# Kernel optimization log

Hardware: AMD Instinct MI355X
Metric: run time of the kernel (lower is better)

## Reference

```python
import jax, jax.numpy as jnp
import numpy as np

DEPTH = 2   # depth
H = 8       # heads
DH = 32     # dim_head
DIM = 256   # model dim (= H*DH)
W = 2       # sliding_window_size
C = 4       # compress_block_size == selection_block_size
NSEL = 2    # num_selected_blocks
B, S = 4, 2048


def layernorm(x, g, b, eps=1e-5):
    m = x.mean(-1, keepdims=True)
    v = jnp.var(x, axis=-1, keepdims=True)
    return (x - m) * jax.lax.rsqrt(v + eps) * g + b


def msoftmax(s, mask):
    # numerically-safe masked softmax; rows with no visible key output zeros
    s = jnp.where(mask, s, -1e9)
    p = jax.nn.softmax(s, axis=-1)
    return jnp.where(jnp.any(mask, axis=-1, keepdims=True), p, 0.0)


def nsa(x, Wq, Wk, Wv, Wg, Wo):
    # Native sparse attention: compressed + top-k selected blocks + sliding window,
    # combined with per-head sigmoid gates.
    b, s, d = x.shape
    nb = s // C
    q = (x @ Wq).reshape(b, s, H, DH).transpose(0, 2, 1, 3)  # [B,H,S,DH]
    k = (x @ Wk).reshape(b, s, H, DH).transpose(0, 2, 1, 3)
    v = (x @ Wv).reshape(b, s, H, DH).transpose(0, 2, 1, 3)
    scale = DH ** -0.5
    t = jnp.arange(s)

    # ---- compressed branch: mean-pooled KV blocks, causal over fully-past blocks
    kb = k.reshape(b, H, nb, C, DH)
    vb = v.reshape(b, H, nb, C, DH)
    kc = kb.mean(3)
    vc = vb.mean(3)
    sc = jnp.einsum('bhsd,bhnd->bhsn', q, kc) * scale       # [B,H,S,nb]
    blk_end = jnp.arange(nb) * C + (C - 1)
    cmask = blk_end[None, :] <= t[:, None]                   # [S,nb]
    pc = msoftmax(sc, cmask[None, None])
    oc = jnp.einsum('bhsn,bhnd->bhsd', pc, vc)

    # ---- selection branch: own block always + top (NSEL-1) blocks by compressed score
    own = t // C                                             # [S]
    not_own = jnp.arange(nb)[None, :] != own[:, None]        # [S,nb]
    sel_scores = jnp.where(not_own[None, None], pc, -1.0)
    top_idx = jax.lax.top_k(sel_scores, NSEL - 1)[1]         # [B,H,S,NSEL-1]
    own_idx = jnp.broadcast_to(own[None, None, :, None], (b, H, s, 1))
    idx = jnp.concatenate([own_idx, top_idx], axis=-1)       # [B,H,S,NSEL]
    idxf = idx.reshape(b, H, s * NSEL, 1, 1)
    sk = jnp.take_along_axis(kb, idxf, axis=2).reshape(b, H, s, NSEL * C, DH)
    sv = jnp.take_along_axis(vb, idxf, axis=2).reshape(b, H, s, NSEL * C, DH)
    pos = (idx[..., None] * C + jnp.arange(C)).reshape(b, H, s, NSEL * C)
    fmask = pos <= t[None, None, :, None]
    sf = jnp.einsum('bhsd,bhskd->bhsk', q, sk) * scale
    pf = msoftmax(sf, fmask)
    of = jnp.einsum('bhsk,bhskd->bhsd', pf, sv)

    # ---- sliding-window branch: causal local window of W tokens (incl. self)
    off = jnp.arange(W) - (W - 1)
    wpos = t[:, None] + off[None, :]                         # [S,W]
    widx = jnp.clip(wpos, 0, s - 1)
    kw = jnp.take(k, widx.reshape(-1), axis=2).reshape(b, H, s, W, DH)
    vw = jnp.take(v, widx.reshape(-1), axis=2).reshape(b, H, s, W, DH)
    sw = jnp.einsum('bhsd,bhsjd->bhsj', q, kw) * scale
    pw = msoftmax(sw, (wpos >= 0)[None, None])
    ow = jnp.einsum('bhsj,bhsjd->bhsd', pw, vw)

    # ---- gated combine + output projection
    g = jax.nn.sigmoid(x @ Wg).reshape(b, s, 3, H).transpose(0, 3, 1, 2)  # [B,H,S,3]
    o = g[..., 0:1] * oc + g[..., 1:2] * of + g[..., 2:3] * ow
    return o.transpose(0, 2, 1, 3).reshape(b, s, H * DH) @ Wo


def forward(x, ln_a_g, ln_a_b, Wq, Wk, Wv, Wg, Wo, ln_f_g, ln_f_b, W1, b1, W2, b2):
    for l in range(DEPTH):
        for j in range(2):  # two attention sub-layers per block
            i = l * 2 + j
            h = layernorm(x, ln_a_g[i], ln_a_b[i])
            x = x + nsa(h, Wq[i], Wk[i], Wv[i], Wg[i], Wo[i])
        h = layernorm(x, ln_f_g[l], ln_f_b[l])
        h = h @ W1[l] + b1[l]
        h = jnp.where(h > 0, h, 0.01 * h)  # LeakyReLU
        x = x + h @ W2[l] + b2[l]
    return x


def setup_inputs() -> dict:
    key = jax.random.key(0)
    ks = jax.random.split(key, 8)
    A = DEPTH * 2
    r = lambda k, shp: jax.random.normal(k, shp, jnp.float32) * 0.02
    return {
        'x': jax.random.normal(ks[0], (B, S, DIM), jnp.float32),
        'ln_a_g': jnp.ones((A, DIM), jnp.float32),
        'ln_a_b': jnp.zeros((A, DIM), jnp.float32),
        'Wq': r(ks[1], (A, DIM, H * DH)),
        'Wk': r(ks[2], (A, DIM, H * DH)),
        'Wv': r(ks[3], (A, DIM, H * DH)),
        'Wg': r(ks[4], (A, DIM, 3 * H)),
        'Wo': r(ks[5], (A, H * DH, DIM)),
        'ln_f_g': jnp.ones((DEPTH, DIM), jnp.float32),
        'ln_f_b': jnp.zeros((DEPTH, DIM), jnp.float32),
        'W1': r(ks[6], (DEPTH, DIM, 2 * DIM)),
        'b1': jnp.zeros((DEPTH, 2 * DIM), jnp.float32),
        'W2': r(ks[7], (DEPTH, 2 * DIM, DIM)),
        'b2': jnp.zeros((DEPTH, DIM), jnp.float32),
    }


def reference(x, ln_a_g, ln_a_b, Wq, Wk, Wv, Wg, Wo, ln_f_g, ln_f_b, W1, b1, W2, b2):
    return forward(x, ln_a_g, ln_a_b, Wq, Wk, Wv, Wg, Wo, ln_f_g, ln_f_b, W1, b1, W2, b2)
```

## Files before the change

kernel.cpp:

```cpp
#include <hip/hip_runtime.h>
#include <hip/hip_bf16.h>
#include <math.h>

#define NH 8
#define DH 32
#define DIM 256
#define SEQ 2048
#define BATCH 4
#define NB 512
#define QKS 512
#define VGS 320
#define SCALE 0.17677669529663687f

typedef short short8v __attribute__((ext_vector_type(8)));
typedef float float4v __attribute__((ext_vector_type(4)));

__device__ __forceinline__ float sigmoidf_(float x){ return 1.f/(1.f+__expf(-x)); }
__device__ __forceinline__ ushort f2bf(float f){
  uint b = __float_as_uint(f);
  return (ushort)((b + 0x7fffu + ((b>>16)&1u)) >> 16);
}
__device__ __forceinline__ float bf2f(ushort u){ return __uint_as_float(((uint)u)<<16); }
__device__ __forceinline__ float bflo(uint u){ return __uint_as_float(u<<16); }
__device__ __forceinline__ float bfhi(uint u){ return __uint_as_float(u & 0xffff0000u); }
__device__ __forceinline__ uint pk2(float a, float b){ return (uint)f2bf(a) | ((uint)f2bf(b)<<16); }
__device__ __forceinline__ void bfu4_to_f32(uint4 u, float* f){
  f[0]=bflo(u.x); f[1]=bfhi(u.x);
  f[2]=bflo(u.y); f[3]=bfhi(u.y);
  f[4]=bflo(u.z); f[5]=bfhi(u.z);
  f[6]=bflo(u.w); f[7]=bfhi(u.w);
}

__global__ void copy_f32(const float* __restrict__ in, float* __restrict__ out, int n4){
  int i = blockIdx.x*blockDim.x + threadIdx.x;
  if (i < n4) ((float4*)out)[i] = ((const float4*)in)[i];
}

__global__ void build_wqk(const float* __restrict__ Wq, const float* __restrict__ Wk, float* __restrict__ out){
  int i = blockIdx.x*256 + threadIdx.x;
  if (i >= 4*256*QKS) return;
  int col = i & 511, rk = (i>>9)&255, l = i>>17;
  out[i] = (col < 256) ? Wq[((size_t)l*256+rk)*256+col] : Wk[((size_t)l*256+rk)*256+col-256];
}
__global__ void build_wvgT(const float* __restrict__ Wv, const float* __restrict__ Wg, ushort* __restrict__ out){
  int i = blockIdx.x*256 + threadIdx.x;
  if (i >= 4*VGS*256) return;
  int k = i & 255, n = (i>>8)%VGS, l = i/(VGS*256);
  float v = 0.f;
  if      (n < 256) v = Wv[((size_t)l*256+k)*256+n];
  else if (n < 280) v = Wg[((size_t)l*256+k)*24 + (n-256)];
  out[i] = f2bf(v);
}
__global__ void build_wT(const float* __restrict__ in, ushort* __restrict__ out, int L, int K, int N){
  int i = blockIdx.x*256 + threadIdx.x;
  if (i >= L*K*N) return;
  int k = i % K, n = (i/K) % N, l = i/(K*N);
  out[i] = f2bf(in[((size_t)l*K+k)*N+n]);
}

__global__ __launch_bounds__(256) void ln_k(const float* __restrict__ x, const float* __restrict__ g,
                                            const float* __restrict__ b, float* __restrict__ h,
                                            ushort* __restrict__ hb){
  int row  = blockIdx.x*4 + (threadIdx.x>>6);
  int lane = threadIdx.x & 63;
  int c = lane*4;
  const float* xr = x + (size_t)row*DIM + c;
  float4 v = *(const float4*)xr;
  float s = v.x+v.y+v.z+v.w;
  float q = v.x*v.x+v.y*v.y+v.z*v.z+v.w*v.w;
  #pragma unroll
  for (int off=32; off>0; off>>=1){ s += __shfl_xor(s, off); q += __shfl_xor(q, off); }
  float mean = s * (1.f/DIM);
  float var  = q * (1.f/DIM) - mean*mean;
  float rs = rsqrtf(var + 1e-5f);
  float4 gg = *(const float4*)(g + c);
  float4 bb = *(const float4*)(b + c);
  float4 o;
  o.x = (v.x-mean)*rs*gg.x + bb.x;
  o.y = (v.y-mean)*rs*gg.y + bb.y;
  o.z = (v.z-mean)*rs*gg.z + bb.z;
  o.w = (v.w-mean)*rs*gg.w + bb.w;
  *(float4*)(h + (size_t)row*DIM + c) = o;
  uint2 u;
  u.x = pk2(o.x, o.y);
  u.y = pk2(o.z, o.w);
  *(uint2*)&hb[(size_t)row*DIM + c] = u;
}

__global__ __launch_bounds__(256) void gemm_qkvg(
    const float* __restrict__ hA, const ushort* __restrict__ hbA,
    const float* __restrict__ Bqk, const ushort* __restrict__ BvgT,
    float* __restrict__ qkb, ushort* __restrict__ vgu,
    float* __restrict__ kcb, ushort* __restrict__ vctb){
  __shared__ __align__(16) char smem[25600];
  int tid = threadIdx.x;
  int m0 = blockIdx.x*128;
  if (blockIdx.y < 8){
    float (*As)[132] = (float(*)[132])smem;
    float (*Bs)[68]  = (float(*)[68])(smem + 16896);
    int n0 = blockIdx.y*64;
    int tx = tid & 15, tyy = tid >> 4;
    int ar = tid >> 1;
    int ac = (tid & 1)*16;
    int bk = tid >> 3;
    int bn = (tid & 7)*8;
    const float* Ap = hA + (size_t)(m0+ar)*256 + ac;
    const float* Bp = Bqk + (size_t)bk*QKS + n0 + bn;
    float4 apre[4], bpre[2];
    #pragma unroll
    for (int j=0;j<4;j++) apre[j] = *(const float4*)(Ap + 4*j);
    bpre[0] = *(const float4*)Bp;
    bpre[1] = *(const float4*)(Bp + 4);
    float acc[8][4];
    #pragma unroll
    for (int i=0;i<8;i++)
      #pragma unroll
      for (int j=0;j<4;j++) acc[i][j]=0.f;
    for (int k0=0; k0<256; k0+=32){
      #pragma unroll
      for (int j=0;j<4;j++){
        As[ac+4*j+0][ar]=apre[j].x; As[ac+4*j+1][ar]=apre[j].y;
        As[ac+4*j+2][ar]=apre[j].z; As[ac+4*j+3][ar]=apre[j].w;
      }
      *(float4*)&Bs[bk][bn]   = bpre[0];
      *(float4*)&Bs[bk][bn+4] = bpre[1];
      __syncthreads();
      if (k0 + 32 < 256){
        #pragma unroll
        for (int j=0;j<4;j++) apre[j] = *(const float4*)(Ap + k0 + 32 + 4*j);
        bpre[0] = *(const float4*)(Bp + (size_t)(k0+32)*QKS);
        bpre[1] = *(const float4*)(Bp + (size_t)(k0+32)*QKS + 4);
      }
      #pragma unroll
      for (int kk=0;kk<32;kk++){
        float4 bv  = *(const float4*)&Bs[kk][tx*4];
        float4 av0 = *(const float4*)&As[kk][tyy*8];
        float4 av1 = *(const float4*)&As[kk][tyy*8+4];
        float av[8] = {av0.x,av0.y,av0.z,av0.w,av1.x,av1.y,av1.z,av1.w};
        float bw[4] = {bv.x,bv.y,bv.z,bv.w};
        #pragma unroll
        for (int i=0;i<8;i++)
          #pragma unroll
          for (int j=0;j<4;j++) acc[i][j] += av[i]*bw[j];
      }
      __syncthreads();
    }
    #pragma unroll
    for (int i=0;i<8;i++){
      int m = m0 + tyy*8 + i;
      #pragma unroll
      for (int j=0;j<4;j++)
        qkb[(size_t)m*QKS + n0 + tx*4 + j] = acc[i][j];
    }
    if (n0 >= 256){
      #pragma unroll
      for (int G=0; G<2; ++G){
        int row = m0 + tyy*8 + 4*G;
        int bi = row >> 11;
        int np = (row & 2047) >> 2;
        #pragma unroll
        for (int j=0;j<4;j++){
          int col = n0 + tx*4 + j - 256;
          int h_ = col >> 5, d = col & 31;
          float pv = 0.25f*(((acc[4*G][j] + acc[4*G+1][j]) + acc[4*G+2][j]) + acc[4*G+3][j]);
          kcb[(((size_t)(bi*NH + h_))*NB + np)*DH + d] = pv;
        }
      }
    }
  } else {
    ushort* Al = (ushort*)smem;
    ushort* Bl = (ushort*)(smem + 16384);
    int n0 = (blockIdx.y - 8)*64;
    int w = tid>>6, lane = tid&63;
    int wm = w>>1, wn = w&1;
    float4v acc[4][2];
    #pragma unroll
    for (int i=0;i<4;i++)
      #pragma unroll
      for (int j=0;j<2;j++) acc[i][j] = (float4v){0.f,0.f,0.f,0.f};
    for (int k0=0; k0<256; k0+=64){
      #pragma unroll
      for (int i=0;i<4;i++){
        int id = tid + 256*i;
        int r = id>>3, c = id&7;
        *(uint4*)&Al[r*64 + ((c ^ (r&7))*8)] = *(const uint4*)&hbA[(size_t)(m0+r)*256 + k0 + c*8];
      }
      #pragma unroll
      for (int i=0;i<2;i++){
        int id = tid + 256*i;
        int r = id>>3, c = id&7;
        *(uint4*)&Bl[r*64 + ((c ^ (r&7))*8)] = *(const uint4*)&BvgT[(size_t)(n0+r)*256 + k0 + c*8];
      }
      __syncthreads();
      #pragma unroll
      for (int kk=0; kk<2; ++kk){
        short8v a[4], bfr[2];
        #pragma unroll
        for (int mf=0; mf<4; mf++){
          int r = wm*64 + mf*16 + (lane&15);
          int c = (kk*4 + (lane>>4)) ^ (r&7);
          a[mf] = *(short8v*)&Al[r*64 + c*8];
        }
        #pragma unroll
        for (int nf=0; nf<2; nf++){
          int r = wn*32 + nf*16 + (lane&15);
          int c = (kk*4 + (lane>>4)) ^ (r&7);
          bfr[nf] = *(short8v*)&Bl[r*64 + c*8];
        }
        #pragma unroll
        for (int mf=0; mf<4; mf++)
          #pragma unroll
          for (int nf=0; nf<2; nf++)
            acc[mf][nf] = __builtin_amdgcn_mfma_f32_16x16x32_bf16(a[mf], bfr[nf], acc[mf][nf], 0, 0, 0);
      }
      __syncthreads();
    }
    #pragma unroll
    for (int nf=0; nf<2; nf++){
      int col = n0 + wn*32 + nf*16 + (lane&15);
      #pragma unroll
      for (int mf=0; mf<4; mf++){
        ushort s4[4];
        #pragma unroll
        for (int r=0; r<4; r++){
          int row = m0 + wm*64 + mf*16 + (lane>>4)*4 + r;
          s4[r] = f2bf(acc[mf][nf][r]);
          vgu[(size_t)row*VGS + col] = s4[r];
        }
        if (col < 256){
          int row0 = m0 + wm*64 + mf*16 + (lane>>4)*4;
          int bi = row0 >> 11;
          int np = (row0 & 2047) >> 2;
          float pv = 0.25f*(((bf2f(s4[0]) + bf2f(s4[1])) + bf2f(s4[2])) + bf2f(s4[3]));
          int h_ = col >> 5, d = col & 31;
          vctb[(((size_t)(bi*NH + h_))*DH + d)*NB + np] = f2bf(pv);
        }
      }
    }
  }
}

template<bool BIAS, bool LEAKY, bool ACC, bool OBF16>
__global__ __launch_bounds__(256) void gemm_bf16(const ushort* __restrict__ A, const ushort* __restrict__ Bt,
                                                 const float* __restrict__ bias, void* __restrict__ Cv,
                                                 int M, int N, int K){
  __shared__ ushort Al[128*64];
  __shared__ ushort Bl[64*64];
  int tid = threadIdx.x;
  int m0 = blockIdx.x*128, n0 = blockIdx.y*64;
  int w = tid>>6, lane = tid&63;
  int wm = w>>1, wn = w&1;
  float4v acc[4][2];
  #pragma unroll
  for (int i=0;i<4;i++)
    #pragma unroll
    for (int j=0;j<2;j++) acc[i][j] = (float4v){0.f,0.f,0.f,0.f};
  for (int k0=0; k0<K; k0+=64){
    #pragma unroll
    for (int i=0;i<4;i++){
      int id = tid + 256*i;
      int r = id>>3, c = id&7;
      *(uint4*)&Al[r*64 + ((c ^ (r&7))*8)] = *(const uint4*)&A[(size_t)(m0+r)*K + k0 + c*8];
    }
    #pragma unroll
    for (int i=0;i<2;i++){
      int id = tid + 256*i;
      int r = id>>3, c = id&7;
      *(uint4*)&Bl[r*64 + ((c ^ (r&7))*8)] = *(const uint4*)&Bt[(size_t)(n0+r)*K + k0 + c*8];
    }
    __syncthreads();
    #pragma unroll
    for (int kk=0; kk<2; ++kk){
      short8v a[4], bfr[2];
      #pragma unroll
      for (int mf=0; mf<4; mf++){
        int r = wm*64 + mf*16 + (lane&15);
        int c = (kk*4 + (lane>>4)) ^ (r&7);
        a[mf] = *(short8v*)&Al[r*64 + c*8];
      }
      #pragma unroll
      for (int nf=0; nf<2; nf++){
        int r = wn*32 + nf*16 + (lane&15);
        int c = (kk*4 + (lane>>4)) ^ (r&7);
        bfr[nf] = *(short8v*)&Bl[r*64 + c*8];
      }
      #pragma unroll
      for (int mf=0; mf<4; mf++)
        #pragma unroll
        for (int nf=0; nf<2; nf++)
          acc[mf][nf] = __builtin_amdgcn_mfma_f32_16x16x32_bf16(a[mf], bfr[nf], acc[mf][nf], 0, 0, 0);
    }
    __syncthreads();
  }
  #pragma unroll
  for (int nf=0; nf<2; nf++){
    int col = n0 + wn*32 + nf*16 + (lane&15);
    float bv = BIAS ? bias[col] : 0.f;
    #pragma unroll
    for (int mf=0; mf<4; mf++){
      #pragma unroll
      for (int r=0; r<4; r++){
        int row = m0 + wm*64 + mf*16 + (lane>>4)*4 + r;
        float vv = acc[mf][nf][r];
        if (BIAS) vv += bv;
        if (LEAKY) vv = vv > 0.f ? vv : 0.01f*vv;
        if (OBF16) ((ushort*)Cv)[(size_t)row*N + col] = f2bf(vv);
        else {
          float* C = (float*)Cv;
          if (ACC) vv += C[(size_t)row*N + col];
          C[(size_t)row*N + col] = vv;
        }
      }
    }
  }
}

__global__ __launch_bounds__(256, 4) void nsa_attn(
    const float* __restrict__ qk, const ushort* __restrict__ vg,
    const float* __restrict__ kc, const ushort* __restrict__ vct,
    ushort* __restrict__ o)
{
  __shared__ float  kt[64*32];
  __shared__ ushort vcT[32*72];
  __shared__ ushort Pl[64*72];
  __shared__ float  ocl[64*36];
  __shared__ float4 meta[4*64];
  int e = blockIdx.x;
  int hh = e & 7;
  int b  = (e >> 3) & 3;
  int qq = (e >> 5) & 7;
  int r  = e >> 8;
  int g  = (r==0) ? (31-qq) : (r==1) ? qq : (r==2) ? (23-qq) : (8+qq);
  int tid = threadIdx.x;
  int w = tid >> 6, lane = tid & 63;
  const float*  kcg  = kc  + ((size_t)(b*NH + hh)*NB)*DH;
  const ushort* vctg = vct + ((size_t)(b*NH + hh)*DH)*NB;

  {
    int t = g*64 + lane;
    int own = t >> 2, nvis = (t+1) >> 2;
    int nmax = 16*(g+1);
    float qv[32];
    {
      const float4* qr = (const float4*)(qk + ((size_t)b*SEQ + t)*QKS + hh*DH);
      #pragma unroll
      for (int d8=0; d8<8; d8++){
        float4 a4 = qr[d8];
        qv[4*d8]=a4.x; qv[4*d8+1]=a4.y; qv[4*d8+2]=a4.z; qv[4*d8+3]=a4.w;
      }
    }
    float l = 0.f, best = -1e30f;
    int bn1 = -1;
    float4v acc0 = (float4v){0.f,0.f,0.f,0.f};
    float4v acc1 = (float4v){0.f,0.f,0.f,0.f};

    int tiles = (g + 4) >> 2;
    for (int ti=0; ti<tiles; ++ti){
      int base = ti*64;
      if (ti) __syncthreads();
      {
        const float4* sk = (const float4*)(kcg + (size_t)base*DH);
        ((float4*)kt)[tid]     = sk[tid];
        ((float4*)kt)[tid+256] = sk[tid+256];
        int sd = tid >> 3, sn = (tid & 7)*8;
        *(uint4*)&vcT[sd*72 + sn] = *(const uint4*)&vctg[(size_t)sd*NB + base + sn];
      }
      __syncthreads();
      float ps[16];
      #pragma unroll
      for (int j=0; j<16; ++j){
        int rr = w*16 + j;
        int n = base + rr;
        float p = 0.f;
        if (n < nmax){
          const float4* kp = (const float4*)&kt[rr*32];
          float s = 0.f;
          #pragma unroll
          for (int d8=0; d8<8; d8++){
            float4 k4 = kp[d8];
            s += qv[4*d8]*k4.x + qv[4*d8+1]*k4.y + qv[4*d8+2]*k4.z + qv[4*d8+3]*k4.w;
          }
          s *= SCALE;
          bool act = (n < nvis);
          if (act && n != own && s > best){ best = s; bn1 = n; }
          p = act ? __expf(s) : 0.f;
          l += p;
        }
        ps[j] = p;
      }
      {
        uint4 u0, u1;
        u0.x = pk2(ps[0],ps[1]);  u0.y = pk2(ps[2],ps[3]);
        u0.z = pk2(ps[4],ps[5]);  u0.w = pk2(ps[6],ps[7]);
        u1.x = pk2(ps[8],ps[9]);  u1.y = pk2(ps[10],ps[11]);
        u1.z = pk2(ps[12],ps[13]);u1.w = pk2(ps[14],ps[15]);
        *(uint4*)&Pl[lane*72 + w*16]     = u0;
        *(uint4*)&Pl[lane*72 + w*16 + 8] = u1;
      }
      __syncthreads();
      #pragma unroll
      for (int ks=0; ks<2; ++ks){
        short8v a  = *(short8v*)&Pl [(16*w + (lane&15))*72 + ks*32 + (lane>>4)*8];
        short8v b0 = *(short8v*)&vcT[(lane&15)*72        + ks*32 + (lane>>4)*8];
        short8v b1 = *(short8v*)&vcT[((lane&15)+16)*72   + ks*32 + (lane>>4)*8];
        acc0 = __builtin_amdgcn_mfma_f32_16x16x32_bf16(a, b0, acc0, 0, 0, 0);
        acc1 = __builtin_amdgcn_mfma_f32_16x16x32_bf16(a, b1, acc1, 0, 0, 0);
      }
    }
    #pragma unroll
    for (int r2=0; r2<4; ++r2){
      int token = 16*w + (lane>>4)*4 + r2;
      ocl[token*36 + (lane&15)]      = acc0[r2];
      ocl[token*36 + 16 + (lane&15)] = acc1[r2];
    }
    meta[w*64 + lane] = make_float4(l, best, __int_as_float(bn1), 0.f);
  }
  __syncthreads();

  {
    int tok = tid >> 2;
    int ds  = (tid & 3)*8;
    int t = g*64 + tok;
    int own = t >> 2, nvis = (t+1) >> 2;
    float q8[8];
    {
      const float4* qr = (const float4*)(qk + ((size_t)b*SEQ + t)*QKS + hh*DH + ds);
      float4 a4 = qr[0], b4 = qr[1];
      q8[0]=a4.x; q8[1]=a4.y; q8[2]=a4.z; q8[3]=a4.w;
      q8[4]=b4.x; q8[5]=b4.y; q8[6]=b4.z; q8[7]=b4.w;
    }
    float out8[8];
    {
      float4 oA = *(const float4*)&ocl[tok*36 + ds];
      float4 oB = *(const float4*)&ocl[tok*36 + ds + 4];
      out8[0]=oA.x; out8[1]=oA.y; out8[2]=oA.z; out8[3]=oA.w;
      out8[4]=oB.x; out8[5]=oB.y; out8[6]=oB.z; out8[7]=oB.w;
    }
    float ll = 0.f, bb = -1e30f;
    int bn = (own==0) ? 1 : 0;
    #pragma unroll
    for (int sp=0; sp<4; ++sp){
      float4 m4 = meta[sp*64 + tok];
      ll += m4.x;
      int mi = __float_as_int(m4.z);
      if (m4.y > bb || (m4.y == bb && mi >= 0 && mi < bn)){ bb = m4.y; bn = mi; }
    }
    const ushort* gr = vg + ((size_t)b*SEQ + t)*VGS + 256;
    float g0 = sigmoidf_(bf2f(gr[hh])), g1 = sigmoidf_(bf2f(gr[8+hh])), g2 = sigmoidf_(bf2f(gr[16+hh]));
    float inv = (nvis > 0) ? g0/ll : 0.f;
    #pragma unroll
    for (int j=0;j<8;j++) out8[j] *= inv;

    const float*  kb2 = qk + (size_t)b*SEQ*QKS + 256 + hh*DH + ds;
    const ushort* vb2 = vg + (size_t)b*SEQ*VGS + hh*DH + ds;
    float s2[8];
    float m2 = -1e30f;
    #pragma unroll
    for (int ki=0; ki<8; ++ki){
      int tt = (ki<4 ? own : bn)*4 + (ki&3);
      float s = -1e30f;
      if (tt <= t){
        const float4* kr = (const float4*)(kb2 + (size_t)tt*QKS);
        float4 a4 = kr[0], c4 = kr[1];
        float ps = q8[0]*a4.x + q8[1]*a4.y + q8[2]*a4.z + q8[3]*a4.w
                 + q8[4]*c4.x + q8[5]*c4.y + q8[6]*c4.z + q8[7]*c4.w;
        ps += __shfl_xor(ps, 1);
        ps += __shfl_xor(ps, 2);
        s = ps*SCALE;
        m2 = fmaxf(m2, s);
      }
      s2[ki] = s;
    }
    float l2 = 0.f;
    #pragma unroll
    for (int ki=0; ki<8; ++ki)
      if (s2[ki] > -1e29f) l2 += __expf(s2[ki] - m2);
    float inv2 = g1/l2;
    #pragma unroll
    for (int ki=0; ki<8; ++ki){
      int tt = (ki<4 ? own : bn)*4 + (ki&3);
      if (tt <= t){
        float pw = __expf(s2[ki] - m2) * inv2;
        uint4 u = *(const uint4*)(vb2 + (size_t)tt*VGS);
        float f[8]; bfu4_to_f32(u, f);
        #pragma unroll
        for (int j=0;j<8;j++) out8[j] += pw*f[j];
      }
    }

    int tp = (t>0) ? t-1 : 0;
    float sa, sb;
    {
      const float4* ka = (const float4*)(kb2 + (size_t)tp*QKS);
      const float4* kb4= (const float4*)(kb2 + (size_t)t *QKS);
      float4 a0 = ka[0], a1 = ka[1], b0 = kb4[0], b1 = kb4[1];
      float pa_ = q8[0]*a0.x + q8[1]*a0.y + q8[2]*a0.z + q8[3]*a0.w
                + q8[4]*a1.x + q8[5]*a1.y + q8[6]*a1.z + q8[7]*a1.w;
      float pb_ = q8[0]*b0.x + q8[1]*b0.y + q8[2]*b0.z + q8[3]*b0.w
                + q8[4]*b1.x + q8[5]*b1.y + q8[6]*b1.z + q8[7]*b1.w;
      pa_ += __shfl_xor(pa_, 1); pa_ += __shfl_xor(pa_, 2);
      pb_ += __shfl_xor(pb_, 1); pb_ += __shfl_xor(pb_, 2);
      sa = pa_*SCALE; sb = pb_*SCALE;
    }
    float m3 = (t>0) ? fmaxf(sa, sb) : sb;
    float pa = (t>0) ? __expf(sa-m3) : 0.f;
    float pb = __expf(sb-m3);
    float inv3 = g2/(pa+pb);
    float va[8], vbv[8];
    bfu4_to_f32(*(const uint4*)(vb2 + (size_t)tp*VGS), va);
    bfu4_to_f32(*(const uint4*)(vb2 + (size_t)t *VGS), vbv);
    ushort* orow = o + ((size_t)b*SEQ + t)*DIM + hh*DH + ds;
    float rr[8];
    #pragma unroll
    for (int j=0;j<8;j++) rr[j] = out8[j] + (pa*va[j] + pb*vbv[j])*inv3;
    uint4 u;
    u.x = pk2(rr[0], rr[1]);
    u.y = pk2(rr[2], rr[3]);
    u.z = pk2(rr[4], rr[5]);
    u.w = pk2(rr[6], rr[7]);
    *(uint4*)orow = u;
  }
}

extern "C" void kernel_launch(void* const* d_in, const int* in_sizes, int n_in,
                              void* d_out, int out_size, void* d_ws, size_t ws_size,
                              hipStream_t stream) {
  const float* x_in   = (const float*)d_in[0];
  const float* ln_a_g = (const float*)d_in[1];
  const float* ln_a_b = (const float*)d_in[2];
  const float* Wq     = (const float*)d_in[3];
  const float* Wk     = (const float*)d_in[4];
  const float* Wv     = (const float*)d_in[5];
  const float* Wg     = (const float*)d_in[6];
  const float* Wo     = (const float*)d_in[7];
  const float* ln_f_g = (const float*)d_in[8];
  const float* ln_f_b = (const float*)d_in[9];
  const float* W1     = (const float*)d_in[10];
  const float* b1     = (const float*)d_in[11];
  const float* W2     = (const float*)d_in[12];
  const float* b2     = (const float*)d_in[13];

  float* xout = (float*)d_out;
  float* ws = (float*)d_ws;
  const size_t NTOK = (size_t)BATCH*SEQ;
  float* h    = ws;
  float* qkb  = h    + NTOK*DIM;
  float* kcb  = qkb  + NTOK*QKS;
  ushort* vctb = (ushort*)(kcb + (size_t)BATCH*NH*NB*DH);
  float* wqk  = (float*)(vctb + (size_t)BATCH*NH*NB*DH);
  ushort* hb   = (ushort*)(wqk + (size_t)4*DIM*QKS);
  ushort* vgu  = hb   + NTOK*DIM;
  ushort* obu  = vgu  + NTOK*VGS;
  ushort* midu = obu  + NTOK*DIM;
  ushort* wvgT = midu + NTOK*512;
  ushort* woT  = wvgT + (size_t)4*VGS*DIM;
  ushort* w1T  = woT  + (size_t)4*DIM*DIM;
  ushort* w2T  = w1T  + (size_t)2*512*DIM;

  copy_f32<<<2048, 256, 0, stream>>>(x_in, xout, (int)(NTOK*DIM/4));
  build_wqk <<<(4*256*QKS+255)/256, 256, 0, stream>>>(Wq, Wk, wqk);
  build_wvgT<<<(4*VGS*256+255)/256, 256, 0, stream>>>(Wv, Wg, wvgT);
  build_wT  <<<(4*256*256+255)/256, 256, 0, stream>>>(Wo, woT, 4, 256, 256);
  build_wT  <<<(2*256*512+255)/256, 256, 0, stream>>>(W1, w1T, 2, 256, 512);
  build_wT  <<<(2*512*256+255)/256, 256, 0, stream>>>(W2, w2T, 2, 512, 256);

  dim3 gfused(64,13), g4(64,4), g8(64,8);
  for (int i=0;i<4;i++){
    ln_k<<<2048,256,0,stream>>>(xout, ln_a_g + i*DIM, ln_a_b + i*DIM, h, hb);
    gemm_qkvg<<<gfused,256,0,stream>>>(h, hb, wqk + (size_t)i*DIM*QKS, wvgT + (size_t)i*VGS*DIM,
                                       qkb, vgu, kcb, vctb);
    nsa_attn<<<1024,256,0,stream>>>(qkb, vgu, kcb, vctb, obu);
    gemm_bf16<false,false,true,false><<<g4,256,0,stream>>>(obu, woT + (size_t)i*DIM*DIM, nullptr, xout, 8192,DIM,256);
    if (i & 1){
      int l = i >> 1;
      ln_k<<<2048,256,0,stream>>>(xout, ln_f_g + l*DIM, ln_f_b + l*DIM, h, hb);
      gemm_bf16<true,true,false,true><<<g8,256,0,stream>>>(hb,   w1T + (size_t)l*512*DIM, b1 + l*512, midu, 8192,512,256);
      gemm_bf16<true,false,true,false><<<g4,256,0,stream>>>(midu, w2T + (size_t)l*DIM*512, b2 + l*DIM, xout, 8192,DIM,512);
    }
  }
}
```

Measured before the change: 507.5 us.

## Keep attention accumulators in registers and use 64x64 tiles for N=256 GEMMs

```diff
diff --git a/kernel.cpp b/kernel.cpp
--- a/kernel.cpp
+++ b/kernel.cpp
@@ -24,11 +24,9 @@
 __device__ __forceinline__ float bflo(uint u){ return __uint_as_float(u<<16); }
 __device__ __forceinline__ float bfhi(uint u){ return __uint_as_float(u & 0xffff0000u); }
 __device__ __forceinline__ uint pk2(float a, float b){ return (uint)f2bf(a) | ((uint)f2bf(b)<<16); }
-__device__ __forceinline__ void bfu4_to_f32(uint4 u, float* f){
+__device__ __forceinline__ void bfu2_to_f32(uint2 u, float* f){
   f[0]=bflo(u.x); f[1]=bfhi(u.x);
   f[2]=bflo(u.y); f[3]=bfhi(u.y);
-  f[4]=bflo(u.z); f[5]=bfhi(u.z);
-  f[6]=bflo(u.w); f[7]=bfhi(u.w);
 }
 
 __global__ void copy_f32(const float* __restrict__ in, float* __restrict__ out, int n4){
@@ -315,6 +313,62 @@
   }
 }
 
+template<bool BIAS, bool LEAKY, bool ACC, bool OBF16>
+__global__ __launch_bounds__(256) void gemm_bf16_64(const ushort* __restrict__ A, const ushort* __restrict__ Bt,
+                                                    const float* __restrict__ bias, void* __restrict__ Cv,
+                                                    int M, int N, int K){
+  __shared__ ushort Al[64*64];
+  __shared__ ushort Bl[64*64];
+  int tid = threadIdx.x;
+  int m0 = blockIdx.x*64, n0 = blockIdx.y*64;
+  int w = tid>>6, lane = tid&63;
+  float4v acc[4];
+  #pragma unroll
+  for (int j=0;j<4;j++) acc[j] = (float4v){0.f,0.f,0.f,0.f};
+  for (int k0=0; k0<K; k0+=64){
+    #pragma unroll
+    for (int i=0;i<2;i++){
+      int id = tid + 256*i;
+      int r = id>>3, c = id&7;
+      *(uint4*)&Al[r*64 + ((c ^ (r&7))*8)] = *(const uint4*)&A[(size_t)(m0+r)*K + k0 + c*8];
+      *(uint4*)&Bl[r*64 + ((c ^ (r&7))*8)] = *(const uint4*)&Bt[(size_t)(n0+r)*K + k0 + c*8];
+    }
+    __syncthreads();
+    #pragma unroll
+    for (int kk=0; kk<2; ++kk){
+      int ra = 16*w + (lane&15);
+      int ca = (kk*4 + (lane>>4)) ^ (ra&7);
+      short8v a = *(short8v*)&Al[ra*64 + ca*8];
+      #pragma unroll
+      for (int nf=0; nf<4; nf++){
+        int rb = nf*16 + (lane&15);
+        int cb = (kk*4 + (lane>>4)) ^ (rb&7);
+        short8v bfr = *(short8v*)&Bl[rb*64 + cb*8];
+        acc[nf] = __builtin_amdgcn_mfma_f32_16x16x32_bf16(a, bfr, acc[nf], 0, 0, 0);
+      }
+    }
+    __syncthreads();
+  }
+  #pragma unroll
+  for (int nf=0; nf<4; nf++){
+    int col = n0 + nf*16 + (lane&15);
+    float bv = BIAS ? bias[col] : 0.f;
+    #pragma unroll
+    for (int r=0; r<4; r++){
+      int row = m0 + 16*w + (lane>>4)*4 + r;
+      float vv = acc[nf][r];
+      if (BIAS) vv += bv;
+      if (LEAKY) vv = vv > 0.f ? vv : 0.01f*vv;
+      if (OBF16) ((ushort*)Cv)[(size_t)row*N + col] = f2bf(vv);
+      else {
+        float* C = (float*)Cv;
+        if (ACC) vv += C[(size_t)row*N + col];
+        C[(size_t)row*N + col] = vv;
+      }
+    }
+  }
+}
+
 __global__ __launch_bounds__(256, 4) void nsa_attn(
     const float* __restrict__ qk, const ushort* __restrict__ vg,
     const float* __restrict__ kc, const ushort* __restrict__ vct,
@@ -323,7 +377,6 @@
   __shared__ float  kt[64*32];
   __shared__ ushort vcT[32*72];
   __shared__ ushort Pl[64*72];
-  __shared__ float  ocl[64*36];
   __shared__ float4 meta[4*64];
   int e = blockIdx.x;
   int hh = e & 7;
@@ -336,6 +389,9 @@
   const float*  kcg  = kc  + ((size_t)(b*NH + hh)*NB)*DH;
   const ushort* vctg = vct + ((size_t)(b*NH + hh)*DH)*NB;
 
+  float4v acc0 = (float4v){0.f,0.f,0.f,0.f};
+  float4v acc1 = (float4v){0.f,0.f,0.f,0.f};
+
   {
     int t = g*64 + lane;
     int own = t >> 2, nvis = (t+1) >> 2;
@@ -351,8 +407,6 @@
     }
     float l = 0.f, best = -1e30f;
     int bn1 = -1;
-    float4v acc0 = (float4v){0.f,0.f,0.f,0.f};
-    float4v acc1 = (float4v){0.f,0.f,0.f,0.f};
 
     int tiles = (g + 4) >> 2;
     for (int ti=0; ti<tiles; ++ti){
@@ -400,47 +454,39 @@
       __syncthreads();
       #pragma unroll
       for (int ks=0; ks<2; ++ks){
-        short8v a  = *(short8v*)&Pl [(16*w + (lane&15))*72 + ks*32 + (lane>>4)*8];
-        short8v b0 = *(short8v*)&vcT[(lane&15)*72        + ks*32 + (lane>>4)*8];
-        short8v b1 = *(short8v*)&vcT[((lane&15)+16)*72   + ks*32 + (lane>>4)*8];
-        acc0 = __builtin_amdgcn_mfma_f32_16x16x32_bf16(a, b0, acc0, 0, 0, 0);
-        acc1 = __builtin_amdgcn_mfma_f32_16x16x32_bf16(a, b1, acc1, 0, 0, 0);
-      }
-    }
-    #pragma unroll
-    for (int r2=0; r2<4; ++r2){
-      int token = 16*w + (lane>>4)*4 + r2;
-      ocl[token*36 + (lane&15)]      = acc0[r2];
-      ocl[token*36 + 16 + (lane&15)] = acc1[r2];
+        short8v bfrag = *(short8v*)&Pl [(16*w + (lane&15))*72 + ks*32 + (lane>>4)*8];
+        short8v a0    = *(short8v*)&vcT[(lane&15)*72          + ks*32 + (lane>>4)*8];
+        short8v a1    = *(short8v*)&vcT[((lane&15)+16)*72     + ks*32 + (lane>>4)*8];
+        acc0 = __builtin_amdgcn_mfma_f32_16x16x32_bf16(a0, bfrag, acc0, 0, 0, 0);
+        acc1 = __builtin_amdgcn_mfma_f32_16x16x32_bf16(a1, bfrag, acc1, 0, 0, 0);
+      }
     }
     meta[w*64 + lane] = make_float4(l, best, __int_as_float(bn1), 0.f);
   }
   __syncthreads();
 
   {
-    int tok = tid >> 2;
-    int ds  = (tid & 3)*8;
-    int t = g*64 + tok;
+    int c = lane & 15, m = lane >> 4;
+    int tokidx = w*16 + c;
+    int t = g*64 + tokidx;
     int own = t >> 2, nvis = (t+1) >> 2;
+    int dA = 4*m, dB = 16 + 4*m;
     float q8[8];
     {
-      const float4* qr = (const float4*)(qk + ((size_t)b*SEQ + t)*QKS + hh*DH + ds);
-      float4 a4 = qr[0], b4 = qr[1];
+      const float* qrow = qk + ((size_t)b*SEQ + t)*QKS + hh*DH;
+      float4 a4 = *(const float4*)(qrow + dA);
+      float4 b4 = *(const float4*)(qrow + dB);
       q8[0]=a4.x; q8[1]=a4.y; q8[2]=a4.z; q8[3]=a4.w;
       q8[4]=b4.x; q8[5]=b4.y; q8[6]=b4.z; q8[7]=b4.w;
     }
     float out8[8];
-    {
-      float4 oA = *(const float4*)&ocl[tok*36 + ds];
-      float4 oB = *(const float4*)&ocl[tok*36 + ds + 4];
-      out8[0]=oA.x; out8[1]=oA.y; out8[2]=oA.z; out8[3]=oA.w;
-      out8[4]=oB.x; out8[5]=oB.y; out8[6]=oB.z; out8[7]=oB.w;
-    }
+    #pragma unroll
+    for (int j=0;j<4;j++){ out8[j] = acc0[j]; out8[4+j] = acc1[j]; }
     float ll = 0.f, bb = -1e30f;
     int bn = (own==0) ? 1 : 0;
     #pragma unroll
     for (int sp=0; sp<4; ++sp){
-      float4 m4 = meta[sp*64 + tok];
+      float4 m4 = meta[sp*64 + tokidx];
       ll += m4.x;
       int mi = __float_as_int(m4.z);
       if (m4.y > bb || (m4.y == bb && mi >= 0 && mi < bn)){ bb = m4.y; bn = mi; }
@@ -451,8 +497,8 @@
     #pragma unroll
     for (int j=0;j<8;j++) out8[j] *= inv;
 
-    const float*  kb2 = qk + (size_t)b*SEQ*QKS + 256 + hh*DH + ds;
-    const ushort* vb2 = vg + (size_t)b*SEQ*VGS + hh*DH + ds;
+    const float*  kb2 = qk + (size_t)b*SEQ*QKS + 256 + hh*DH;
+    const ushort* vb2 = vg + (size_t)b*SEQ*VGS + hh*DH;
     float s2[8];
     float m2 = -1e30f;
     #pragma unroll
@@ -460,12 +506,13 @@
       int tt = (ki<4 ? own : bn)*4 + (ki&3);
       float s = -1e30f;
       if (tt <= t){
-        const float4* kr = (const float4*)(kb2 + (size_t)tt*QKS);
-        float4 a4 = kr[0], c4 = kr[1];
+        const float* kr = kb2 + (size_t)tt*QKS;
+        float4 a4 = *(const float4*)(kr + dA);
+        float4 c4 = *(const float4*)(kr + dB);
         float ps = q8[0]*a4.x + q8[1]*a4.y + q8[2]*a4.z + q8[3]*a4.w
                  + q8[4]*c4.x + q8[5]*c4.y + q8[6]*c4.z + q8[7]*c4.w;
-        ps += __shfl_xor(ps, 1);
-        ps += __shfl_xor(ps, 2);
+        ps += __shfl_xor(ps, 16);
+        ps += __shfl_xor(ps, 32);
         s = ps*SCALE;
         m2 = fmaxf(m2, s);
       }
@@ -481,44 +528,50 @@
       int tt = (ki<4 ? own : bn)*4 + (ki&3);
       if (tt <= t){
         float pw = __expf(s2[ki] - m2) * inv2;
-        uint4 u = *(const uint4*)(vb2 + (size_t)tt*VGS);
-        float f[8]; bfu4_to_f32(u, f);
-        #pragma unroll
-        for (int j=0;j<8;j++) out8[j] += pw*f[j];
+        float fA[4], fB[4];
+        bfu2_to_f32(*(const uint2*)(vb2 + (size_t)tt*VGS + dA), fA);
+        bfu2_to_f32(*(const uint2*)(vb2 + (size_t)tt*VGS + dB), fB);
+        #pragma unroll
+        for (int j=0;j<4;j++){ out8[j] += pw*fA[j]; out8[4+j] += pw*fB[j]; }
       }
     }
 
     int tp = (t>0) ? t-1 : 0;
     float sa, sb;
     {
-      const float4* ka = (const float4*)(kb2 + (size_t)tp*QKS);
-      const float4* kb4= (const float4*)(kb2 + (size_t)t *QKS);
-      float4 a0 = ka[0], a1 = ka[1], b0 = kb4[0], b1 = kb4[1];
+      const float* ka = kb2 + (size_t)tp*QKS;
+      const float* kb4= kb2 + (size_t)t *QKS;
+      float4 a0 = *(const float4*)(ka + dA), a1 = *(const float4*)(ka + dB);
+      float4 b0 = *(const float4*)(kb4 + dA), b1 = *(const float4*)(kb4 + dB);
       float pa_ = q8[0]*a0.x + q8[1]*a0.y + q8[2]*a0.z + q8[3]*a0.w
                 + q8[4]*a1.x + q8[5]*a1.y + q8[6]*a1.z + q8[7]*a1.w;
       float pb_ = q8[0]*b0.x + q8[1]*b0.y + q8[2]*b0.z + q8[3]*b0.w
                 + q8[4]*b1.x + q8[5]*b1.y + q8[6]*b1.z + q8[7]*b1.w;
-      pa_ += __shfl_xor(pa_, 1); pa_ += __shfl_xor(pa_, 2);
-      pb_ += __shfl_xor(pb_, 1); pb_ += __shfl_xor(pb_, 2);
+      pa_ += __shfl_xor(pa_, 16); pa_ += __shfl_xor(pa_, 32);
+      pb_ += __shfl_xor(pb_, 16); pb_ += __shfl_xor(pb_, 32);
       sa = pa_*SCALE; sb = pb_*SCALE;
     }
     float m3 = (t>0) ? fmaxf(sa, sb) : sb;
     float pa = (t>0) ? __expf(sa-m3) : 0.f;
     float pb = __expf(sb-m3);
     float inv3 = g2/(pa+pb);
-    float va[8], vbv[8];
-    bfu4_to_f32(*(const uint4*)(vb2 + (size_t)tp*VGS), va);
-    bfu4_to_f32(*(const uint4*)(vb2 + (size_t)t *VGS), vbv);
-    ushort* orow = o + ((size_t)b*SEQ + t)*DIM + hh*DH + ds;
-    float rr[8];
-    #pragma unroll
-    for (int j=0;j<8;j++) rr[j] = out8[j] + (pa*va[j] + pb*vbv[j])*inv3;
-    uint4 u;
-    u.x = pk2(rr[0], rr[1]);
-    u.y = pk2(rr[2], rr[3]);
-    u.z = pk2(rr[4], rr[5]);
-    u.w = pk2(rr[6], rr[7]);
-    *(uint4*)orow = u;
+    float va[4], vaB[4], vbv[4], vbB[4];
+    bfu2_to_f32(*(const uint2*)(vb2 + (size_t)tp*VGS + dA), va);
+    bfu2_to_f32(*(const uint2*)(vb2 + (size_t)tp*VGS + dB), vaB);
+    bfu2_to_f32(*(const uint2*)(vb2 + (size_t)t *VGS + dA), vbv);
+    bfu2_to_f32(*(const uint2*)(vb2 + (size_t)t *VGS + dB), vbB);
+    ushort* orow = o + ((size_t)b*SEQ + t)*DIM + hh*DH;
+    float rrA[4], rrB[4];
+    #pragma unroll
+    for (int j=0;j<4;j++){
+      rrA[j] = out8[j]   + (pa*va[j]  + pb*vbv[j])*inv3;
+      rrB[j] = out8[4+j] + (pa*vaB[j] + pb*vbB[j])*inv3;
+    }
+    uint2 uA, uB;
+    uA.x = pk2(rrA[0], rrA[1]); uA.y = pk2(rrA[2], rrA[3]);
+    uB.x = pk2(rrB[0], rrB[1]); uB.y = pk2(rrB[2], rrB[3]);
+    *(uint2*)&orow[dA] = uA;
+    *(uint2*)&orow[dB] = uB;
   }
 }
 
@@ -564,18 +617,18 @@
   build_wT  <<<(2*256*512+255)/256, 256, 0, stream>>>(W1, w1T, 2, 256, 512);
   build_wT  <<<(2*512*256+255)/256, 256, 0, stream>>>(W2, w2T, 2, 512, 256);
 
-  dim3 gfused(64,13), g4(64,4), g8(64,8);
+  dim3 gfused(64,13), g64(128,4), g8(64,8);
   for (int i=0;i<4;i++){
     ln_k<<<2048,256,0,stream>>>(xout, ln_a_g + i*DIM, ln_a_b + i*DIM, h, hb);
     gemm_qkvg<<<gfused,256,0,stream>>>(h, hb, wqk + (size_t)i*DIM*QKS, wvgT + (size_t)i*VGS*DIM,
                                        qkb, vgu, kcb, vctb);
     nsa_attn<<<1024,256,0,stream>>>(qkb, vgu, kcb, vctb, obu);
-    gemm_bf16<false,false,true,false><<<g4,256,0,stream>>>(obu, woT + (size_t)i*DIM*DIM, nullptr, xout, 8192,DIM,256);
+    gemm_bf16_64<false,false,true,false><<<g64,256,0,stream>>>(obu, woT + (size_t)i*DIM*DIM, nullptr, xout, 8192,DIM,256);
     if (i & 1){
       int l = i >> 1;
       ln_k<<<2048,256,0,stream>>>(xout, ln_f_g + l*DIM, ln_f_b + l*DIM, h, hb);
       gemm_bf16<true,true,false,true><<<g8,256,0,stream>>>(hb,   w1T + (size_t)l*512*DIM, b1 + l*512, midu, 8192,512,256);
-      gemm_bf16<true,false,true,false><<<g4,256,0,stream>>>(midu, w2T + (size_t)l*DIM*512, b2 + l*DIM, xout, 8192,DIM,512);
-    }
-  }
-}
+      gemm_bf16_64<true,false,true,false><<<g64,256,0,stream>>>(midu, w2T + (size_t)l*DIM*512, b2 + l*DIM, xout, 8192,DIM,512);
+    }
+  }
+}
```

Result: slower. 518.9 us (+2.2%).
